# Kernel tuning notes

Hardware: AMD Instinct MI355X
Metric: run time of the kernel (lower is better)

Reference implementation:

```python
import jax, jax.numpy as jnp
import numpy as np

N_HEADS = 8
TANH_CLIP = 10.0
NEG = -1e9  # finite stand-in for -inf so log_softmax/vjp stay NaN-free


def setup_inputs() -> dict:
    key = jax.random.key(0)
    ks = jax.random.split(key, 8)
    B, N, D = 256, 1000, 128
    embeddings = jax.random.normal(ks[0], (B, N, D), dtype=jnp.float32)
    W_node = jax.random.normal(ks[1], (D, 3 * D), dtype=jnp.float32) * (1.0 / np.sqrt(D))
    W_fixed = jax.random.normal(ks[2], (D, D), dtype=jnp.float32) * (1.0 / np.sqrt(D))
    W_step = jax.random.normal(ks[3], (2 * D, D), dtype=jnp.float32) * (1.0 / np.sqrt(2 * D))
    W_out = jax.random.normal(ks[4], (D, D), dtype=jnp.float32) * (1.0 / np.sqrt(D))
    first_idx = jax.random.randint(ks[5], (B,), 0, N)
    last_idx = jax.random.randint(ks[6], (B,), 0, N)
    mask = jax.random.randint(ks[7], (B, N), 0, 2).astype(jnp.bool_)
    mask = mask.at[:, 0].set(False)  # guarantee at least one feasible node
    return {"embeddings": embeddings, "W_node": W_node, "W_fixed": W_fixed,
            "W_step": W_step, "W_out": W_out, "first_idx": first_idx,
            "last_idx": last_idx, "mask": mask}


def reference(embeddings, W_node, W_fixed, W_step, W_out, first_idx, last_idx, mask):
    # One pointer-network decode step (TSP variant of AttentionModel._get_log_p),
    # including the _precompute projections.
    B, N, D = embeddings.shape
    H = N_HEADS
    dk = D // H

    # _precompute: fixed context + glimpse K/V + logit key
    graph_embed = embeddings.mean(axis=1)                       # [B, D]
    fixed_ctx = graph_embed @ W_fixed                           # [B, D]
    kvl = embeddings @ W_node                                   # [B, N, 3D]
    K, V, logit_K = jnp.split(kvl, 3, axis=-1)                  # each [B, N, D]

    # step context: cat(first-node emb, last-node emb) -> project to D
    b = jnp.arange(B)
    step_ctx = jnp.concatenate([embeddings[b, first_idx], embeddings[b, last_idx]], axis=-1)  # [B, 2D]
    q = fixed_ctx + step_ctx @ W_step                           # [B, D]

    # masked multi-head glimpse attention (q_len = 1)
    qh = q.reshape(B, H, dk)                                    # [B, H, dk]
    Kh = K.reshape(B, N, H, dk)
    Vh = V.reshape(B, N, H, dk)
    compat = jnp.einsum('bhd,bnhd->bhn', qh, Kh) / np.sqrt(dk)  # [B, H, N]
    compat = jnp.where(mask[:, None, :], NEG, compat)           # mask_inner
    attn = jax.nn.softmax(compat, axis=-1)
    heads = jnp.einsum('bhn,bnhd->bhd', attn, Vh)               # [B, H, dk]
    glimpse = heads.reshape(B, D) @ W_out                       # [B, D]

    # single-head logit attention with tanh clipping
    logits = jnp.einsum('bd,bnd->bn', glimpse, logit_K) / np.sqrt(D)  # [B, N]
    logits = jnp.tanh(logits) * TANH_CLIP
    logits = jnp.where(mask, NEG, logits)                       # mask_logits
    return jax.nn.log_softmax(logits, axis=-1)                  # [B, N]
```

## Files before the change

kernel.cpp:

```cpp
#include <hip/hip_runtime.h>


#define NEG (-1e9f)

__global__ __launch_bounds__(1024) void k_fused(
    const float* __restrict__ E, const float* __restrict__ Wn,
    const float* __restrict__ Wf, const float* __restrict__ Ws,
    const float* __restrict__ Wo,
    const int* __restrict__ fi, const int* __restrict__ li,
    const int* __restrict__ maskI, const unsigned char* __restrict__ maskB,
    float* __restrict__ out)
{
    const int b = blockIdx.x;
    const int t = threadIdx.x;

    __shared__ float4 Et[4096];
    __shared__ float4 qk4[256];
    __shared__ float4 pt4[256];
    __shared__ float4 EbarF4[256];
    __shared__ float4 mu4[32], e14[32], e24[32], gp4[32];
    __shared__ float q[128], heads[128], gl[128];
    __shared__ float qred[8][128];
    __shared__ float ct[128 * 9];
    __shared__ float mh[8], lh[8], al[8];
    __shared__ float red[16];
    __shared__ float stat[2];
    __shared__ int flagS;

    float* const mu = (float*)mu4;
    float* const e1 = (float*)e14;
    float* const e2 = (float*)e24;
    float* const gp = (float*)gp4;
    float* const pt = (float*)pt4;
    float* const EbarF = (float*)EbarF4;
    float* const qkf = (float*)qk4;

    const float4* E4 = (const float4*)(E + (size_t)b * 128000);

    if (t == 0) flagS = 0;
    const uint4 dv = ((const uint4*)maskI)[t];
    const unsigned det = (dv.x | dv.y | dv.z | dv.w) & 0xFFFFFF00u;

    const int rr = t >> 3, qq = t & 7;
    const int c4 = t & 31, sl = t >> 5;

    {
        const int cm = t & 31, sm = t >> 5;
        float4 acc = make_float4(0.f, 0.f, 0.f, 0.f);
        for (int r = sm; r < 1000; r += 32) {
            const float4 v = E4[r * 32 + cm];
            acc.x += v.x; acc.y += v.y; acc.z += v.z; acc.w += v.w;
        }
        Et[t] = acc;
    }
    if (t >= 512 && t < 544) {
        e14[t - 512] = E4[fi[b] * 32 + (t - 512)];
    } else if (t >= 544 && t < 576) {
        e24[t - 544] = E4[li[b] * 32 + (t - 544)];
    }
    __syncthreads();
    if (det) atomicOr(&flagS, 1);
    if (t < 32) {
        float4 acc = Et[t];
        #pragma unroll
        for (int s = 1; s < 32; ++s) {
            const float4 v = Et[s * 32 + t];
            acc.x += v.x; acc.y += v.y; acc.z += v.z; acc.w += v.w;
        }
        const float inv = 1.0f / 1000.0f;
        mu4[t] = make_float4(acc.x * inv, acc.y * inv, acc.z * inv, acc.w * inv);
    }
    __syncthreads();

    {
        const int part = t >> 7, d = t & 127;
        float acc = 0.f;
        const int k0 = part * 48;
        for (int k = k0; k < k0 + 48; ++k) {
            const float s = (k < 128) ? mu[k] : (k < 256 ? e1[k - 128] : e2[k - 256]);
            const float w = (k < 128) ? Wf[k * 128 + d] : Ws[(k - 128) * 128 + d];
            acc += s * w;
        }
        qred[part][d] = acc;
    }
    __syncthreads();
    if (t < 128) {
        float acc = 0.f;
        #pragma unroll
        for (int p = 0; p < 8; ++p) acc += qred[p][t];
        q[t] = acc;
    }
    __syncthreads();
    {
        const int j = t & 127, cg = t >> 7;
        const float qj = q[j];
        for (int c0 = 0; c0 < 128; c0 += 8) {
            const int c = c0 + cg;
            float v = Wn[c * 384 + j] * qj;
            v += __shfl_down(v, 8, 16);
            v += __shfl_down(v, 4, 16);
            v += __shfl_down(v, 2, 16);
            v += __shfl_down(v, 1, 16);
            if ((j & 15) == 0) {
                const int h = j >> 4, s = c >> 2;
                qkf[h * 128 + (s ^ (s >> 2)) * 4 + (c & 3)] = v * 0.25f;
            }
        }
    }
    if (t < 8) { mh[t] = -3e38f; lh[t] = 0.f; }
    __syncthreads();

    const bool useB = (flagS != 0);

    float4 eacc[8];
    #pragma unroll
    for (int h = 0; h < 8; ++h) eacc[h] = make_float4(0.f, 0.f, 0.f, 0.f);

    for (int tile = 0; tile < 8; ++tile) {
        {
            const int g = tile * 128 + rr;
            float4 v[4];
            if (g < 1000) {
                #pragma unroll
                for (int i = 0; i < 4; ++i) v[i] = E4[g * 32 + qq * 4 + i];
            } else {
                #pragma unroll
                for (int i = 0; i < 4; ++i) v[i] = make_float4(0.f, 0.f, 0.f, 0.f);
            }
            float pch[8];
            #pragma unroll
            for (int h = 0; h < 8; ++h) pch[h] = 0.f;
            #pragma unroll
            for (int i = 0; i < 4; ++i) {
                const int grp = qq * 4 + i;
                Et[rr * 32 + (grp ^ (rr & 7))] = v[i];
                const int sg = grp ^ (grp >> 2);
                #pragma unroll
                for (int h = 0; h < 8; ++h) {
                    const float4 w = qk4[h * 32 + sg];
                    pch[h] += v[i].x * w.x + v[i].y * w.y + v[i].z * w.z + v[i].w * w.w;
                }
            }
            #pragma unroll
            for (int m = 1; m <= 4; m <<= 1) {
                #pragma unroll
                for (int h = 0; h < 8; ++h) pch[h] += __shfl_xor(pch[h], m, 64);
            }
            bool msk = (g >= 1000);
            if (!msk) msk = useB ? (maskB[b * 1000 + g] != 0)
                                 : (maskI[b * 1000 + g] != 0);
            ct[rr * 9 + qq] = msk ? NEG : pch[qq];
        }
        __syncthreads();
        if (t < 64) {
            const int h = t >> 3, j = t & 7;
            float mt = -3e38f;
            for (int r = j; r < 128; r += 8) mt = fmaxf(mt, ct[r * 9 + h]);
            mt = fmaxf(mt, __shfl_xor(mt, 1, 64));
            mt = fmaxf(mt, __shfl_xor(mt, 2, 64));
            mt = fmaxf(mt, __shfl_xor(mt, 4, 64));
            if (j == 0) {
                const float mnew = fmaxf(mh[h], mt);
                al[h] = __expf(mh[h] - mnew);
                mh[h] = mnew;
            }
        }
        __syncthreads();
        {
            float alr[8], mhr[8];
            #pragma unroll
            for (int h = 0; h < 8; ++h) { alr[h] = al[h]; mhr[h] = mh[h]; }
            #pragma unroll
            for (int h = 0; h < 8; ++h) {
                eacc[h].x *= alr[h]; eacc[h].y *= alr[h];
                eacc[h].z *= alr[h]; eacc[h].w *= alr[h];
            }
            #pragma unroll
            for (int j2 = 0; j2 < 4; ++j2) {
                const int r = sl * 4 + j2;
                const float4 ev = Et[r * 32 + (c4 ^ (r & 7))];
                float p[8];
                #pragma unroll
                for (int h = 0; h < 8; ++h) p[h] = __expf(ct[r * 9 + h] - mhr[h]);
                #pragma unroll
                for (int h = 0; h < 8; ++h) {
                    eacc[h].x += p[h] * ev.x; eacc[h].y += p[h] * ev.y;
                    eacc[h].z += p[h] * ev.z; eacc[h].w += p[h] * ev.w;
                }
            }
        }
        if (t < 64) {
            const int h = t >> 3, j = t & 7;
            const float mhh = mh[h];
            float s = 0.f;
            for (int r = j; r < 128; r += 8) s += __expf(ct[r * 9 + h] - mhh);
            s += __shfl_xor(s, 1, 64);
            s += __shfl_xor(s, 2, 64);
            s += __shfl_xor(s, 4, 64);
            if (j == 0) lh[h] = lh[h] * al[h] + s;
        }
        __syncthreads();
    }

    if (sl >= 16) {
        #pragma unroll
        for (int h = 0; h < 8; ++h) Et[(sl - 16) * 256 + h * 32 + c4] = eacc[h];
    }
    __syncthreads();
    if (sl < 16) {
        #pragma unroll
        for (int h = 0; h < 8; ++h) {
            const float4 o = Et[sl * 256 + h * 32 + c4];
            eacc[h].x += o.x; eacc[h].y += o.y; eacc[h].z += o.z; eacc[h].w += o.w;
            Et[sl * 256 + h * 32 + c4] = eacc[h];
        }
    }
    __syncthreads();
    if (t < 256) {
        const int h = t >> 5, cc = t & 31;
        float4 s = make_float4(0.f, 0.f, 0.f, 0.f);
        #pragma unroll
        for (int s2 = 0; s2 < 16; ++s2) {
            const float4 v = Et[s2 * 256 + h * 32 + cc];
            s.x += v.x; s.y += v.y; s.z += v.z; s.w += v.w;
        }
        const float invl = 1.0f / lh[h];
        EbarF4[h * 32 + cc] = make_float4(s.x * invl, s.y * invl, s.z * invl, s.w * invl);
    }
    __syncthreads();

    {
        const int part = t >> 7, d = t & 127, h = d >> 4;
        float acc = 0.f;
        const int c0 = part * 16;
        for (int c = c0; c < c0 + 16; ++c) acc += EbarF[h * 128 + c] * Wn[c * 384 + 128 + d];
        qred[part][d] = acc;
    }
    __syncthreads();
    if (t < 128) {
        float acc = 0.f;
        #pragma unroll
        for (int p = 0; p < 8; ++p) acc += qred[p][t];
        heads[t] = acc;
    }
    __syncthreads();
    {
        const int part = t >> 7, d = t & 127;
        float acc = 0.f;
        const int j0 = part * 16;
        for (int j = j0; j < j0 + 16; ++j) acc += heads[j] * Wo[j * 128 + d];
        qred[part][d] = acc;
    }
    __syncthreads();
    if (t < 128) {
        float acc = 0.f;
        #pragma unroll
        for (int p = 0; p < 8; ++p) acc += qred[p][t];
        gl[t] = acc;
    }
    __syncthreads();
    {
        const int part = t >> 7, c = t & 127;
        float acc = 0.f;
        const int d0 = part * 16;
        for (int d = d0; d < d0 + 16; ++d) acc += Wn[c * 384 + 256 + d] * gl[d];
        qred[part][c] = acc;
    }
    __syncthreads();
    if (t < 128) {
        float acc = 0.f;
        #pragma unroll
        for (int p = 0; p < 8; ++p) acc += qred[p][t];
        gp[t] = acc * 0.08838834764831845f;
    }
    __syncthreads();

    for (int tile = 0; tile < 8; ++tile) {
        const int g = tile * 128 + rr;
        float acc = 0.f;
        if (g < 1000) {
            #pragma unroll
            for (int i = 0; i < 4; ++i) {
                const float4 v = E4[g * 32 + qq * 4 + i];
                const float4 w = gp4[qq * 4 + i];
                acc += v.x * w.x + v.y * w.y + v.z * w.z + v.w * w.w;
            }
        }
        acc += __shfl_xor(acc, 1, 64);
        acc += __shfl_xor(acc, 2, 64);
        acc += __shfl_xor(acc, 4, 64);
        if (qq == 0 && g < 1000) {
            float zz = 10.0f * tanhf(acc);
            const bool m = useB ? (maskB[b * 1000 + g] != 0)
                                : (maskI[b * 1000 + g] != 0);
            if (m) zz = NEG;
            pt[g] = zz;
        }
    }
    __syncthreads();
    float v = (t < 1000) ? pt[t] : -3e38f;
    #pragma unroll
    for (int off = 32; off > 0; off >>= 1) v = fmaxf(v, __shfl_down(v, off, 64));
    if ((t & 63) == 0) red[t >> 6] = v;
    __syncthreads();
    if (t == 0) {
        float m = red[0];
        for (int i = 1; i < 16; ++i) m = fmaxf(m, red[i]);
        stat[0] = m;
    }
    __syncthreads();
    float sv = (t < 1000) ? __expf(pt[t] - stat[0]) : 0.f;
    #pragma unroll
    for (int off = 32; off > 0; off >>= 1) sv += __shfl_down(sv, off, 64);
    if ((t & 63) == 0) red[t >> 6] = sv;
    __syncthreads();
    if (t == 0) {
        float s = 0.f;
        for (int i = 0; i < 16; ++i) s += red[i];
        stat[1] = stat[0] + __logf(s);
    }
    __syncthreads();
    if (t < 1000)
        out[(size_t)b * 1000 + t] = pt[t] - stat[1];
}

extern "C" void kernel_launch(void* const* d_in, const int* in_sizes, int n_in,
                              void* d_out, int out_size, void* d_ws, size_t ws_size,
                              hipStream_t stream) {
    const float* E  = (const float*)d_in[0];
    const float* Wn = (const float*)d_in[1];
    const float* Wf = (const float*)d_in[2];
    const float* Ws = (const float*)d_in[3];
    const float* Wo = (const float*)d_in[4];
    const int*   fi = (const int*)d_in[5];
    const int*   li = (const int*)d_in[6];
    const int*   maskI = (const int*)d_in[7];
    const unsigned char* maskB = (const unsigned char*)d_in[7];
    float* out = (float*)d_out;

    k_fused<<<256, 1024, 0, stream>>>(E, Wn, Wf, Ws, Wo, fi, li, maskI, maskB, out);
}
```

Baseline: 304.1 us.

## Use per-wave online softmax state to drop block barriers in glimpse loop

Each wave now keeps its own running max and sum per head in registers. The reductions use cross-lane shuffles and readfirstlane instead of shared-memory ct/mh/al arrays and three __syncthreads per tile. Softmax weights go to a small per-wave buffer in shared memory, ordered with a local waitcnt, since each wave only reads the rows it wrote. After the loop, the per-wave states are merged once through shared memory and the partial accumulators are rescaled. This removes the 1024-thread block barriers and the serial 64-thread phases from every tile. In exchange it adds redundant exp work per wave and relies on implicit wave-level ordering of LDS accesses.

```diff
diff --git a/kernel.cpp b/kernel.cpp
--- a/kernel.cpp
+++ b/kernel.cpp
@@ -2,6 +2,10 @@
 
 
 #define NEG (-1e9f)
+
+__device__ __forceinline__ float rfl(float x) {
+    return __int_as_float(__builtin_amdgcn_readfirstlane(__float_as_int(x)));
+}
 
 __global__ __launch_bounds__(1024) void k_fused(
     const float* __restrict__ E, const float* __restrict__ Wn,
@@ -21,8 +25,7 @@
     __shared__ float4 mu4[32], e14[32], e24[32], gp4[32];
     __shared__ float q[128], heads[128], gl[128];
     __shared__ float qred[8][128];
-    __shared__ float ct[128 * 9];
-    __shared__ float mh[8], lh[8], al[8];
+    __shared__ float mh[8], lh[8];
     __shared__ float red[16];
     __shared__ float stat[2];
     __shared__ int flagS;
@@ -34,6 +37,7 @@
     float* const pt = (float*)pt4;
     float* const EbarF = (float*)EbarF4;
     float* const qkf = (float*)qk4;
+    float* const qrf = (float*)qred;
 
     const float4* E4 = (const float4*)(E + (size_t)b * 128000);
 
@@ -43,6 +47,7 @@
 
     const int rr = t >> 3, qq = t & 7;
     const int c4 = t & 31, sl = t >> 5;
+    const int wv = t >> 6;
 
     {
         const int cm = t & 31, sm = t >> 5;
@@ -107,18 +112,23 @@
             }
         }
     }
-    if (t < 8) { mh[t] = -3e38f; lh[t] = 0.f; }
     __syncthreads();
 
     const bool useB = (flagS != 0);
 
+    float s_m[8], s_l[8];
+    #pragma unroll
+    for (int h = 0; h < 8; ++h) { s_m[h] = -3e38f; s_l[h] = 0.f; }
     float4 eacc[8];
     #pragma unroll
     for (int h = 0; h < 8; ++h) eacc[h] = make_float4(0.f, 0.f, 0.f, 0.f);
 
     for (int tile = 0; tile < 8; ++tile) {
+        const int g = tile * 128 + rr;
+        float pch[8];
+        #pragma unroll
+        for (int h = 0; h < 8; ++h) pch[h] = 0.f;
         {
-            const int g = tile * 128 + rr;
             float4 v[4];
             if (g < 1000) {
                 #pragma unroll
@@ -127,9 +137,6 @@
                 #pragma unroll
                 for (int i = 0; i < 4; ++i) v[i] = make_float4(0.f, 0.f, 0.f, 0.f);
             }
-            float pch[8];
-            #pragma unroll
-            for (int h = 0; h < 8; ++h) pch[h] = 0.f;
             #pragma unroll
             for (int i = 0; i < 4; ++i) {
                 const int grp = qq * 4 + i;
@@ -141,66 +148,103 @@
                     pch[h] += v[i].x * w.x + v[i].y * w.y + v[i].z * w.z + v[i].w * w.w;
                 }
             }
+        }
+        #pragma unroll
+        for (int m = 1; m <= 4; m <<= 1) {
             #pragma unroll
-            for (int m = 1; m <= 4; m <<= 1) {
-                #pragma unroll
-                for (int h = 0; h < 8; ++h) pch[h] += __shfl_xor(pch[h], m, 64);
-            }
-            bool msk = (g >= 1000);
-            if (!msk) msk = useB ? (maskB[b * 1000 + g] != 0)
-                                 : (maskI[b * 1000 + g] != 0);
-            ct[rr * 9 + qq] = msk ? NEG : pch[qq];
-        }
-        __syncthreads();
-        if (t < 64) {
-            const int h = t >> 3, j = t & 7;
-            float mt = -3e38f;
-            for (int r = j; r < 128; r += 8) mt = fmaxf(mt, ct[r * 9 + h]);
-            mt = fmaxf(mt, __shfl_xor(mt, 1, 64));
-            mt = fmaxf(mt, __shfl_xor(mt, 2, 64));
-            mt = fmaxf(mt, __shfl_xor(mt, 4, 64));
-            if (j == 0) {
-                const float mnew = fmaxf(mh[h], mt);
-                al[h] = __expf(mh[h] - mnew);
-                mh[h] = mnew;
-            }
-        }
-        __syncthreads();
-        {
-            float alr[8], mhr[8];
+            for (int h = 0; h < 8; ++h) pch[h] += __shfl_xor(pch[h], m, 64);
+        }
+        bool msk = (g >= 1000);
+        if (!msk) msk = useB ? (maskB[b * 1000 + g] != 0)
+                             : (maskI[b * 1000 + g] != 0);
+        if (msk) {
             #pragma unroll
-            for (int h = 0; h < 8; ++h) { alr[h] = al[h]; mhr[h] = mh[h]; }
-            #pragma unroll
-            for (int h = 0; h < 8; ++h) {
-                eacc[h].x *= alr[h]; eacc[h].y *= alr[h];
-                eacc[h].z *= alr[h]; eacc[h].w *= alr[h];
-            }
-            #pragma unroll
-            for (int j2 = 0; j2 < 4; ++j2) {
-                const int r = sl * 4 + j2;
-                const float4 ev = Et[r * 32 + (c4 ^ (r & 7))];
-                float p[8];
-                #pragma unroll
-                for (int h = 0; h < 8; ++h) p[h] = __expf(ct[r * 9 + h] - mhr[h]);
-                #pragma unroll
-                for (int h = 0; h < 8; ++h) {
-                    eacc[h].x += p[h] * ev.x; eacc[h].y += p[h] * ev.y;
-                    eacc[h].z += p[h] * ev.z; eacc[h].w += p[h] * ev.w;
-                }
-            }
-        }
-        if (t < 64) {
-            const int h = t >> 3, j = t & 7;
-            const float mhh = mh[h];
-            float s = 0.f;
-            for (int r = j; r < 128; r += 8) s += __expf(ct[r * 9 + h] - mhh);
-            s += __shfl_xor(s, 1, 64);
-            s += __shfl_xor(s, 2, 64);
-            s += __shfl_xor(s, 4, 64);
-            if (j == 0) lh[h] = lh[h] * al[h] + s;
-        }
-        __syncthreads();
-    }
+            for (int h = 0; h < 8; ++h) pch[h] = NEG;
+        }
+        float al[8];
+        #pragma unroll
+        for (int h = 0; h < 8; ++h) {
+            float x = pch[h];
+            x = fmaxf(x, __shfl_xor(x, 8, 64));
+            x = fmaxf(x, __shfl_xor(x, 16, 64));
+            x = fmaxf(x, __shfl_xor(x, 32, 64));
+            const float mn = rfl(fmaxf(s_m[h], x));
+            al[h] = __expf(s_m[h] - mn);
+            s_m[h] = mn;
+        }
+        float e[8];
+        #pragma unroll
+        for (int h = 0; h < 8; ++h) {
+            e[h] = __expf(pch[h] - s_m[h]);
+            float x = e[h];
+            x += __shfl_xor(x, 8, 64);
+            x += __shfl_xor(x, 16, 64);
+            x += __shfl_xor(x, 32, 64);
+            s_l[h] = rfl(s_l[h] * al[h] + x);
+        }
+        if (qq == 0)      pt4[rr * 2]     = make_float4(e[0], e[1], e[2], e[3]);
+        else if (qq == 1) pt4[rr * 2 + 1] = make_float4(e[4], e[5], e[6], e[7]);
+        asm volatile("s_waitcnt lgkmcnt(0)" ::: "memory");
+        #pragma unroll
+        for (int h = 0; h < 8; ++h) {
+            eacc[h].x *= al[h]; eacc[h].y *= al[h];
+            eacc[h].z *= al[h]; eacc[h].w *= al[h];
+        }
+        #pragma unroll
+        for (int j = 0; j < 4; ++j) {
+            const int r = sl * 4 + j;
+            const float4 ev = Et[r * 32 + (c4 ^ (r & 7))];
+            const float4 p0 = pt4[r * 2];
+            const float4 p1 = pt4[r * 2 + 1];
+            eacc[0].x += p0.x * ev.x; eacc[0].y += p0.x * ev.y; eacc[0].z += p0.x * ev.z; eacc[0].w += p0.x * ev.w;
+            eacc[1].x += p0.y * ev.x; eacc[1].y += p0.y * ev.y; eacc[1].z += p0.y * ev.z; eacc[1].w += p0.y * ev.w;
+            eacc[2].x += p0.z * ev.x; eacc[2].y += p0.z * ev.y; eacc[2].z += p0.z * ev.z; eacc[2].w += p0.z * ev.w;
+            eacc[3].x += p0.w * ev.x; eacc[3].y += p0.w * ev.y; eacc[3].z += p0.w * ev.z; eacc[3].w += p0.w * ev.w;
+            eacc[4].x += p1.x * ev.x; eacc[4].y += p1.x * ev.y; eacc[4].z += p1.x * ev.z; eacc[4].w += p1.x * ev.w;
+            eacc[5].x += p1.y * ev.x; eacc[5].y += p1.y * ev.y; eacc[5].z += p1.y * ev.z; eacc[5].w += p1.y * ev.w;
+            eacc[6].x += p1.z * ev.x; eacc[6].y += p1.z * ev.y; eacc[6].z += p1.z * ev.z; eacc[6].w += p1.z * ev.w;
+            eacc[7].x += p1.w * ev.x; eacc[7].y += p1.w * ev.y; eacc[7].z += p1.w * ev.z; eacc[7].w += p1.w * ev.w;
+        }
+        asm volatile("" ::: "memory");
+    }
+
+    if ((t & 63) == 0) {
+        #pragma unroll
+        for (int h = 0; h < 8; ++h) {
+            qrf[wv * 32 + h] = s_m[h];
+            qrf[wv * 32 + 8 + h] = s_l[h];
+        }
+    }
+    __syncthreads();
+    if (t < 8) {
+        float m = qrf[t];
+        for (int w2 = 1; w2 < 16; ++w2) m = fmaxf(m, qrf[w2 * 32 + t]);
+        mh[t] = m;
+    }
+    __syncthreads();
+    if (t < 128) {
+        const int w2 = t >> 3, h = t & 7;
+        const float f = __expf(qrf[w2 * 32 + h] - mh[h]);
+        qrf[w2 * 32 + 16 + h] = f;
+        qrf[w2 * 32 + 24 + h] = qrf[w2 * 32 + 8 + h] * f;
+    }
+    __syncthreads();
+    if (t < 8) {
+        float s = 0.f;
+        for (int w2 = 0; w2 < 16; ++w2) s += qrf[w2 * 32 + 24 + t];
+        lh[t] = s;
+    }
+    {
+        float fw[8];
+        #pragma unroll
+        for (int h = 0; h < 8; ++h) fw[h] = qrf[wv * 32 + 16 + h];
+        #pragma unroll
+        for (int h = 0; h < 8; ++h) {
+            eacc[h].x *= fw[h]; eacc[h].y *= fw[h];
+            eacc[h].z *= fw[h]; eacc[h].w *= fw[h];
+        }
+    }
+    __syncthreads();
 
     if (sl >= 16) {
         #pragma unroll
```

Result: faster. 288.4 us (-5.2%).
